# Optimization experiments

Measured on AMD Instinct MI355X. Metric: run time of the kernel, lower is better.

The kernel has to match this reference:

```python
import jax, jax.numpy as jnp
from jax import lax
import numpy as np

# ---- static config (matches init_kwargs) ----
B, H, W = 8, 32, 32
L = H * W                      # 1024 tokens
D_MODEL = 384
MAMBA_DIM = 192                # d_model * d_mamba_ratio
LOCAL_DIM = 192
D_INNER = 384                  # expand_m * MAMBA_DIM
D_STATE = 16
D_CONV = 4
DT_RANK = 12                   # ceil(MAMBA_DIM / 16)
NDIR = 4                       # h, h_flip, v, v_flip
RED = 48                       # int(D_INNER * 0.125), BiAttn reduce dim
INNER_C = 192                  # LOCAL_DIM * expand_c
K_C = 8                        # local block depthwise kernel size


def setup_inputs() -> dict:
    key = jax.random.key(0)
    ks = jax.random.split(key, 16)
    s = 0.02
    return {
        "x": jax.random.normal(ks[0], (B, L, D_MODEL), jnp.float32),
        "in_proj_w": jax.random.normal(ks[1], (2 * D_INNER, MAMBA_DIM)) * s,
        "A_log": jnp.broadcast_to(jnp.log(jnp.arange(1, D_STATE + 1, dtype=jnp.float32)), (NDIR, D_INNER, D_STATE)) + 0.0,
        "conv_w": jax.random.normal(ks[2], (NDIR, D_INNER, D_CONV)) * 0.2,
        "conv_b": jax.random.normal(ks[3], (NDIR, D_INNER)) * 0.02,
        "xproj_w": jax.random.normal(ks[4], (NDIR, DT_RANK + 2 * D_STATE, D_INNER)) * s,
        "dtproj_w": jax.random.normal(ks[5], (NDIR, D_INNER, DT_RANK)) * (DT_RANK ** -0.5),
        "dtproj_b": jax.random.normal(ks[6], (NDIR, D_INNER)) * 0.5 - 4.0,
        "Dp": jnp.ones((NDIR, D_INNER)),
        "out_proj_w": jax.random.normal(ks[7], (MAMBA_DIM, D_INNER)) * s,
        "attn_ln_g": jnp.ones((D_INNER,)),
        "attn_ln_b": jnp.zeros((D_INNER,)),
        "attn_gr_w": jax.random.normal(ks[8], (RED, D_INNER)) * s,
        "attn_gr_b": jnp.zeros((RED,)),
        "attn_cs_w": jax.random.normal(ks[9], (D_INNER, RED)) * s,
        "attn_cs_b": jnp.zeros((D_INNER,)),
        "pw1_w": jax.random.normal(ks[10], (2 * INNER_C, LOCAL_DIM)) * s,
        "pw1_b": jnp.zeros((2 * INNER_C,)),
        "dw_w": jax.random.normal(ks[11], (INNER_C, K_C)) * 0.2,
        "dw_b": jnp.zeros((INNER_C,)),
        "bn_g": jnp.ones((INNER_C,)),
        "bn_b": jnp.zeros((INNER_C,)),
        "pw2_w": jax.random.normal(ks[12], (LOCAL_DIM, INNER_C)) * s,
        "pw2_b": jnp.zeros((LOCAL_DIM,)),
    }


def _forward(x, in_proj_w, A_log, conv_w, conv_b, xproj_w, dtproj_w, dtproj_b, Dp,
             out_proj_w, attn_ln_g, attn_ln_b, attn_gr_w, attn_gr_b, attn_cs_w, attn_cs_b,
             pw1_w, pw1_b, dw_w, dw_b, bn_g, bn_b, pw2_w, pw2_b):
    mamba_in = x[:, :, :MAMBA_DIM]
    local_in = x[:, :, MAMBA_DIM:]

    # ---------- MultiMamba branch ----------
    xz = jnp.swapaxes(mamba_in @ in_proj_w.T, 1, 2)   # (B, 2*D_INNER, L)

    def to_dir(t, i):
        # reorder channel-last-token axis per scan direction
        if i == 0:
            return t
        if i == 1:
            return jnp.flip(t, -1)
        tv = t.reshape(B, -1, H, W).swapaxes(-1, -2).reshape(B, -1, L)  # column-major scan
        return tv if i == 2 else jnp.flip(tv, -1)

    def from_dir(t, i):
        if i == 0:
            return t
        if i == 1:
            return jnp.flip(t, -1)
        if i == 3:
            t = jnp.flip(t, -1)
        return t.reshape(B, -1, W, H).swapaxes(-1, -2).reshape(B, -1, L)

    def ssm_dir(xzd, i):
        # mamba_inner_fn_no_out_proj: causal dwconv -> silu -> x_proj -> selective scan -> gate
        xp, z = jnp.split(xzd, 2, axis=1)            # (B, D_INNER, L) each
        xpad = jnp.pad(xp, ((0, 0), (0, 0), (D_CONV - 1, 0)))
        u = lax.conv_general_dilated(xpad, conv_w[i][:, None, :], (1,), 'VALID',
                                     dimension_numbers=('NCH', 'OIH', 'NCH'),
                                     feature_group_count=D_INNER)
        u = jax.nn.silu(u + conv_b[i][None, :, None])
        dbl = jnp.einsum('bdl,rd->brl', u, xproj_w[i])
        dt = dbl[:, :DT_RANK]
        Bm = dbl[:, DT_RANK:DT_RANK + D_STATE]
        Cm = dbl[:, DT_RANK + D_STATE:]
        delta = jax.nn.softplus(jnp.einsum('brl,dr->bdl', dt, dtproj_w[i]) + dtproj_b[i][None, :, None])
        A = -jnp.exp(A_log[i])                        # (D_INNER, D_STATE)

        def step(h, inps):
            d_t, B_t, C_t, u_t = inps                 # (B,d),(B,n),(B,n),(B,d)
            h = jnp.exp(d_t[:, :, None] * A) * h + (d_t * u_t)[:, :, None] * B_t[:, None, :]
            return h, jnp.einsum('bdn,bn->bd', h, C_t)

        h0 = jnp.zeros((B, D_INNER, D_STATE), x.dtype)
        _, ys = lax.scan(step, h0, (delta.transpose(2, 0, 1), Bm.transpose(2, 0, 1),
                                    Cm.transpose(2, 0, 1), u.transpose(2, 0, 1)))
        y = ys.transpose(1, 2, 0) + u * Dp[i][:, None]  # (B, D_INNER, L)
        return y * jax.nn.silu(z)

    def biattn(t):                                     # (B, L, D_INNER)
        mu = t.mean(-1, keepdims=True)
        var = ((t - mu) ** 2).mean(-1, keepdims=True)
        tn = (t - mu) / jnp.sqrt(var + 1e-5) * attn_ln_g + attn_ln_b
        g = tn.mean(1, keepdims=True)                  # global pool (B,1,D_INNER)
        g = jax.nn.gelu(g @ attn_gr_w.T + attn_gr_b, approximate=False)
        c = jax.nn.sigmoid(g @ attn_cs_w.T + attn_cs_b)
        return t * c

    acc = jnp.zeros((B, L, D_INNER), x.dtype)
    for i in range(NDIR):                              # fixed small set of directions
        out_i = from_dir(ssm_dir(to_dir(xz, i), i), i)
        acc = acc + biattn(jnp.swapaxes(out_i, 1, 2))
    mamba_out = acc @ out_proj_w.T                     # (B, L, MAMBA_DIM)

    # ---------- Local conv branch ----------
    hch = jnp.einsum('blc,oc->bol', local_in, pw1_w) + pw1_b[None, :, None]
    a, gte = jnp.split(hch, 2, axis=1)
    hch = a * jax.nn.sigmoid(gte)                      # GLU, (B, INNER_C, L)
    pad_l = K_C // 2
    pad_r = K_C // 2 - (K_C + 1) % 2                   # calc_same_padding(8) -> (4, 3)
    hpad = jnp.pad(hch, ((0, 0), (0, 0), (pad_l, pad_r)))
    hch = lax.conv_general_dilated(hpad, dw_w[:, None, :], (1,), 'VALID',
                                   dimension_numbers=('NCH', 'OIH', 'NCH'),
                                   feature_group_count=INNER_C) + dw_b[None, :, None]
    mu = hch.mean((0, 2))                              # BatchNorm1d (training-mode batch stats)
    var = hch.var((0, 2))
    hch = (hch - mu[None, :, None]) / jnp.sqrt(var + 1e-5)[None, :, None] * bn_g[None, :, None] + bn_b[None, :, None]
    hch = hch * jax.nn.sigmoid(hch)                    # Swish
    local_out = jnp.einsum('bcl,oc->blo', hch, pw2_w) + pw2_b

    return jnp.concatenate([mamba_out, local_out], axis=-1)


def reference(x, in_proj_w, A_log, conv_w, conv_b, xproj_w, dtproj_w, dtproj_b, Dp,
              out_proj_w, attn_ln_g, attn_ln_b, attn_gr_w, attn_gr_b, attn_cs_w, attn_cs_b,
              pw1_w, pw1_b, dw_w, dw_b, bn_g, bn_b, pw2_w, pw2_b):
    return _forward(x, in_proj_w, A_log, conv_w, conv_b, xproj_w, dtproj_w, dtproj_b, Dp,
                    out_proj_w, attn_ln_g, attn_ln_b, attn_gr_w, attn_gr_b, attn_cs_w, attn_cs_b,
                    pw1_w, pw1_b, dw_w, dw_b, bn_g, bn_b, pw2_w, pw2_b)
```

## Files before the change

kernel.cpp:

```cpp
#include <hip/hip_runtime.h>
#include <stdint.h>


#define DEV __device__ __forceinline__

typedef __attribute__((ext_vector_type(8))) short short8;
typedef __attribute__((ext_vector_type(4))) short short4v;
typedef __attribute__((ext_vector_type(4))) float f32x4;

DEV float bf(ushort v) { union { uint32_t u; float f; } c; c.u = ((uint32_t)v) << 16; return c.f; }
DEV ushort fbf(float f) {
  union { float f; uint32_t u; } c; c.f = f;
  uint32_t u = c.u;
  return (ushort)((u + 0x7FFFu + ((u >> 16) & 1u)) >> 16);
}

#if __has_builtin(__builtin_amdgcn_exp2f)
DEV float fexp2(float x) { return __builtin_amdgcn_exp2f(x); }
#else
DEV float fexp2(float x) { return __expf(x * 0.6931471805599453f); }
#endif

template<int CTRL>
DEV float rradd(float x) {
  return x + __int_as_float(__builtin_amdgcn_update_dpp(
      0, __float_as_int(x), CTRL, 0xF, 0xF, true));
}

DEV int pmap(int i, int j) {
  if (i == 0) return j;
  if (i == 1) return 1023 - j;
  if (i == 2) return ((j & 31) << 5) | (j >> 5);
  int k = 1023 - j; return ((k & 31) << 5) | (k >> 5);
}

DEV void cvt4(const float* __restrict__ s, ushort* __restrict__ d, int blk, int tid) {
  const int idx = (blk * 256 + tid) * 4;
  float4 v = *(const float4*)(s + idx);
  d[idx] = fbf(v.x); d[idx + 1] = fbf(v.y); d[idx + 2] = fbf(v.z); d[idx + 3] = fbf(v.w);
}

__global__ __launch_bounds__(256) void prep_all(
    const float* __restrict__ x, ushort* __restrict__ xb,
    const float* __restrict__ ipw, ushort* __restrict__ ipwb,
    const float* __restrict__ opw, ushort* __restrict__ opwb,
    const float* __restrict__ pw1w, ushort* __restrict__ pw1wb,
    const float* __restrict__ pw2w, ushort* __restrict__ pw2wb,
    const float* __restrict__ xw, ushort* __restrict__ xwp)
{
  const int bx = blockIdx.x, tid = threadIdx.x;
  if (bx < 3072)      cvt4(x, xb, bx, tid);
  else if (bx < 3216) cvt4(ipw, ipwb, bx - 3072, tid);
  else if (bx < 3288) cvt4(opw, opwb, bx - 3216, tid);
  else if (bx < 3360) cvt4(pw1w, pw1wb, bx - 3288, tid);
  else if (bx < 3396) cvt4(pw2w, pw2wb, bx - 3360, tid);
  else {
    const int row = bx - 3396;
    const int i = row >> 6, nn = row & 63;
    for (int c = tid; c < 384; c += 256)
      xwp[(size_t)row * 384 + c] = (nn < 44) ? fbf(xw[((size_t)i * 44 + nn) * 384 + c]) : (ushort)0;
  }
}

template<bool BF16OUT, bool BIAS>
__global__ __launch_bounds__(256) void gemm_bt(
    const ushort* __restrict__ A, long long sAz, int lda,
    const ushort* __restrict__ Bw, long long sBz,
    const float* __restrict__ bias,
    void* __restrict__ C, long long sCz, int ldc, int coff, int K)
{
  __shared__ ushort As[64][40];
  __shared__ ushort Bs[64][40];
  A += (size_t)blockIdx.z * sAz;
  Bw += (size_t)blockIdx.z * sBz;
  const int tid = threadIdx.x;
  const int m0 = blockIdx.x * 64, n0 = blockIdx.y * 64;
  const int w = tid >> 6, lane = tid & 63, l15 = lane & 15, quad = lane >> 4;
  const int sr = tid >> 2, sc = (tid & 3) * 8;
  f32x4 acc[4] = {};
  for (int k0 = 0; k0 < K; k0 += 32) {
    __syncthreads();
    *(short8*)&As[sr][sc] = *(const short8*)(A + (size_t)(m0 + sr) * lda + k0 + sc);
    *(short8*)&Bs[sr][sc] = *(const short8*)(Bw + (size_t)(n0 + sr) * K + k0 + sc);
    __syncthreads();
    short8 av = *(short8*)&As[w * 16 + l15][quad * 8];
#pragma unroll
    for (int nt = 0; nt < 4; nt++) {
      short8 bv = *(short8*)&Bs[nt * 16 + l15][quad * 8];
      acc[nt] = __builtin_amdgcn_mfma_f32_16x16x32_bf16(av, bv, acc[nt], 0, 0, 0);
    }
  }
  float* cf = (float*)C + (size_t)blockIdx.z * sCz;
  ushort* cb = (ushort*)C + (size_t)blockIdx.z * sCz;
#pragma unroll
  for (int nt = 0; nt < 4; nt++) {
    const int col = n0 + nt * 16 + l15;
    const float bv = BIAS ? bias[col] : 0.f;
#pragma unroll
    for (int r = 0; r < 4; r++) {
      const int row = m0 + w * 16 + quad * 4 + r;
      float v = acc[nt][r] + bv;
      if (BF16OUT) cb[(size_t)row * ldc + coff + col] = fbf(v);
      else         cf[(size_t)row * ldc + coff + col] = v;
    }
  }
}

__global__ __launch_bounds__(256) void gemm_dual(
    const ushort* __restrict__ A0, int lda0, const ushort* __restrict__ B0,
    const float* __restrict__ bias0, void* __restrict__ C0, int ldc0, int coff0, int K0,
    int nt0, int bf0,
    const ushort* __restrict__ A1, int lda1, const ushort* __restrict__ B1,
    const float* __restrict__ bias1, void* __restrict__ C1, int ldc1, int coff1, int K1,
    int bf1, float* __restrict__ bnsum)
{
  __shared__ ushort As[64][40];
  __shared__ ushort Bs[64][40];
  if (blockIdx.x == 0 && blockIdx.y == 0) {
    for (int k = threadIdx.x; k < 384; k += 256) bnsum[k] = 0.f;
  }
  const ushort* A; const ushort* Bw; const float* bias; void* C;
  int lda, ldc, coff, K, bf16o, n0;
  if ((int)blockIdx.y < nt0) {
    A = A0; lda = lda0; Bw = B0; bias = bias0; C = C0; ldc = ldc0; coff = coff0; K = K0;
    bf16o = bf0; n0 = blockIdx.y * 64;
  } else {
    A = A1; lda = lda1; Bw = B1; bias = bias1; C = C1; ldc = ldc1; coff = coff1; K = K1;
    bf16o = bf1; n0 = (blockIdx.y - nt0) * 64;
  }
  const int tid = threadIdx.x;
  const int m0 = blockIdx.x * 64;
  const int w = tid >> 6, lane = tid & 63, l15 = lane & 15, quad = lane >> 4;
  const int sr = tid >> 2, sc = (tid & 3) * 8;
  f32x4 acc[4] = {};
  for (int k0 = 0; k0 < K; k0 += 32) {
    __syncthreads();
    *(short8*)&As[sr][sc] = *(const short8*)(A + (size_t)(m0 + sr) * lda + k0 + sc);
    *(short8*)&Bs[sr][sc] = *(const short8*)(Bw + (size_t)(n0 + sr) * K + k0 + sc);
    __syncthreads();
    short8 av = *(short8*)&As[w * 16 + l15][quad * 8];
#pragma unroll
    for (int nt = 0; nt < 4; nt++) {
      short8 bv = *(short8*)&Bs[nt * 16 + l15][quad * 8];
      acc[nt] = __builtin_amdgcn_mfma_f32_16x16x32_bf16(av, bv, acc[nt], 0, 0, 0);
    }
  }
#pragma unroll
  for (int nt = 0; nt < 4; nt++) {
    const int col = n0 + nt * 16 + l15;
    const float bv = bias ? bias[col] : 0.f;
#pragma unroll
    for (int r = 0; r < 4; r++) {
      const int row = m0 + w * 16 + quad * 4 + r;
      float v = acc[nt][r] + bv;
      if (bf16o) ((ushort*)C)[(size_t)row * ldc + coff + col] = fbf(v);
      else       ((float*)C)[(size_t)row * ldc + coff + col] = v;
    }
  }
}

__global__ __launch_bounds__(256) void gemm_pw2(
    const float* __restrict__ h2, const float* __restrict__ bnsum,
    const float* __restrict__ bng, const float* __restrict__ bnb,
    const ushort* __restrict__ Bw, const float* __restrict__ bias,
    float* __restrict__ C)
{
  __shared__ ushort As[64][40];
  __shared__ ushort Bs[64][40];
  __shared__ float bsc[192], bsh[192];
  const int tid = threadIdx.x;
  const int m0 = blockIdx.x * 64, n0 = blockIdx.y * 64;
  const int w = tid >> 6, lane = tid & 63, l15 = lane & 15, quad = lane >> 4;
  const int sr = tid >> 2, sc = (tid & 3) * 8;
  for (int cth = tid; cth < 192; cth += 256) {
    float m = bnsum[cth] * (1.f / 8192.f);
    float va = bnsum[192 + cth] * (1.f / 8192.f) - m * m;
    float s = bng[cth] * rsqrtf(va + 1e-5f);
    bsc[cth] = s; bsh[cth] = bnb[cth] - m * s;
  }
  f32x4 acc[4] = {};
  for (int k0 = 0; k0 < 192; k0 += 32) {
    __syncthreads();
    {
      const float* hr = h2 + (size_t)(m0 + sr) * 192 + k0 + sc;
      f32x4 a0 = *(const f32x4*)(hr);
      f32x4 a1 = *(const f32x4*)(hr + 4);
      short8 v;
#pragma unroll
      for (int k = 0; k < 8; k++) {
        const float xx = (k < 4) ? a0[k] : a1[k - 4];
        const float xn = xx * bsc[k0 + sc + k] + bsh[k0 + sc + k];
        v[k] = (short)fbf(xn / (1.f + __expf(-xn)));
      }
      *(short8*)&As[sr][sc] = v;
    }
    *(short8*)&Bs[sr][sc] = *(const short8*)(Bw + (size_t)(n0 + sr) * 192 + k0 + sc);
    __syncthreads();
    short8 av = *(short8*)&As[w * 16 + l15][quad * 8];
#pragma unroll
    for (int nt = 0; nt < 4; nt++) {
      short8 bv = *(short8*)&Bs[nt * 16 + l15][quad * 8];
      acc[nt] = __builtin_amdgcn_mfma_f32_16x16x32_bf16(av, bv, acc[nt], 0, 0, 0);
    }
  }
#pragma unroll
  for (int nt = 0; nt < 4; nt++) {
    const int col = n0 + nt * 16 + l15;
    const float bv = bias[col];
#pragma unroll
    for (int r = 0; r < 4; r++) {
      const int row = m0 + w * 16 + quad * 4 + r;
      C[(size_t)row * 384 + 192 + col] = acc[nt][r] + bv;
    }
  }
}

__global__ __launch_bounds__(256) void convdbl_kernel(
    const ushort* __restrict__ xzb, const float* __restrict__ cw,
    const float* __restrict__ cb, const ushort* __restrict__ xwp,
    ushort* __restrict__ u, float* __restrict__ dbl)
{
  __shared__ __align__(16) ushort sxz[67][392];
  __shared__ float swt[384][4];
  __shared__ float scb[384];
  const int tid = threadIdx.x;
  const int i = blockIdx.y;
  const int m0 = blockIdx.x * 64;
  const int b = m0 >> 10, j0 = m0 & 1023;

  for (int k = tid; k < 1536; k += 256) ((float*)swt)[k] = cw[(size_t)i * 1536 + k];
  for (int k = tid; k < 384; k += 256) scb[k] = cb[i * 384 + k];
  for (int g = tid; g < 67 * 96; g += 256) {
    const int rr = g / 96, c4 = (g % 96) * 4;
    const int jj = j0 - 3 + rr;
    short4v v = {};
    if (jj >= 0)
      v = *(const short4v*)(xzb + (size_t)((b << 10) + pmap(i, jj)) * 768 + c4);
    *(short4v*)&sxz[rr][c4] = v;
  }
  __syncthreads();
  {
    const int r = tid >> 2, cp = tid & 3;
    ushort* ur = u + ((size_t)((i * 8 + b) << 10) + j0 + r) * 384 + cp * 96;
#pragma unroll 4
    for (int q = 0; q < 24; q++) {
      const int c = cp * 96 + q * 4;
      const short4v x0 = *(const short4v*)&sxz[r + 0][c];
      const short4v x1 = *(const short4v*)&sxz[r + 1][c];
      const short4v x2 = *(const short4v*)&sxz[r + 2][c];
      const short4v x3 = *(const short4v*)&sxz[r + 3][c];
      short4v o;
#pragma unroll
      for (int j = 0; j < 4; j++) {
        const f32x4 wv = *(const f32x4*)&swt[c + j][0];
        float s = bf((ushort)x0[j]) * wv[0] + bf((ushort)x1[j]) * wv[1]
                + bf((ushort)x2[j]) * wv[2] + bf((ushort)x3[j]) * wv[3] + scb[c + j];
        o[j] = (short)fbf(s / (1.f + __expf(-s)));
      }
      *(short4v*)(ur + q * 4) = o;
    }
  }
  ushort (*As)[40] = (ushort(*)[40])&sxz[0][0];
  ushort (*Bs)[40] = (ushort(*)[40])(&sxz[0][0] + 2560);
  const ushort* Au = u + (size_t)i * 8192 * 384;
  const ushort* Bw = xwp + (size_t)i * 64 * 384;
  const int w = tid >> 6, lane = tid & 63, l15 = lane & 15, quad = lane >> 4;
  const int sr = tid >> 2, sc = (tid & 3) * 8;
  f32x4 acc[4] = {};
  for (int k0 = 0; k0 < 384; k0 += 32) {
    __syncthreads();
    *(short8*)&As[sr][sc] = *(const short8*)(Au + (size_t)(m0 + sr) * 384 + k0 + sc);
    *(short8*)&Bs[sr][sc] = *(const short8*)(Bw + (size_t)sr * 384 + k0 + sc);
    __syncthreads();
    short8 av = *(short8*)&As[w * 16 + l15][quad * 8];
#pragma unroll
    for (int nt = 0; nt < 4; nt++) {
      short8 bv = *(short8*)&Bs[nt * 16 + l15][quad * 8];
      acc[nt] = __builtin_amdgcn_mfma_f32_16x16x32_bf16(av, bv, acc[nt], 0, 0, 0);
    }
  }
  float* cf = dbl + (size_t)i * 8192 * 64;
#pragma unroll
  for (int nt = 0; nt < 4; nt++) {
    const int col = nt * 16 + l15;
#pragma unroll
    for (int r = 0; r < 4; r++) {
      const int row = m0 + w * 16 + quad * 4 + r;
      cf[(size_t)row * 64 + col] = acc[nt][r];
    }
  }
}

#define NCH 16
#define CJ 64
__global__ __launch_bounds__(256, 3) void scan9_kernel(
    const ushort* __restrict__ u,
    const float*  __restrict__ dbl,
    const ushort* __restrict__ xzb,
    const float* __restrict__ alog, const float* __restrict__ dtw,
    const float* __restrict__ dtb, const float* __restrict__ Dpw,
    ushort* __restrict__ y)
{
  const int dt0 = blockIdx.x * NCH;
  const int b = blockIdx.y, i = blockIdx.z;
  const int tid = threadIdx.x;
  const int ch = tid >> 4, n = tid & 15;
  const int srow = tid >> 2, role = tid & 3;

  __shared__ float sbc[CJ / 2][68];
  __shared__ float sdu[CJ / 2][68];
  __shared__ float sy[CJ][20];
  __shared__ float sDp[NCH];

  float w48[4][12], dtbv4[4];
#pragma unroll
  for (int cc = 0; cc < 4; cc++) {
    const int chp = 4 * role + cc;
#pragma unroll
    for (int r = 0; r < 12; r++) w48[cc][r] = dtw[((size_t)i * 384 + dt0 + chp) * 12 + r];
    dtbv4[cc] = dtb[i * 384 + dt0 + chp];
  }
  const float L2E = 1.4426950408889634f;
  const float Al = -__expf(alog[((size_t)i * 384 + dt0 + ch) * 16 + n]) * L2E;
  if (tid < NCH) sDp[tid] = Dpw[i * 384 + dt0 + tid];

  const float selm[4] = { (n >> 2) == 0 ? 1.f : 0.f, (n >> 2) == 1 ? 1.f : 0.f,
                          (n >> 2) == 2 ? 1.f : 0.f, (n >> 2) == 3 ? 1.f : 0.f };

  const size_t rb = (size_t)(i * 8 + b) << 10;
  const ushort* ub = u + rb * 384 + dt0;
  const float* dblb = dbl + rb * 64;
  const ushort* zb = xzb + ((size_t)b << 10) * 768 + 384 + dt0;
  ushort* yb = y + rb * 384 + dt0;
  const float* sdup = &sdu[0][4 * ch];
  const float* sbcp = &sbc[0][4 * n];

  f32x4 nd0, nd1, nd2, ns0, ns1, ns2; short4v nu, nz;
  {
    const float* src = dblb + (size_t)srow * 64;
    nd0 = *(const f32x4*)(src); nd1 = *(const f32x4*)(src + 4); nd2 = *(const f32x4*)(src + 8);
    const float* seg = src + role * 12;
    ns0 = *(const f32x4*)(seg); ns1 = *(const f32x4*)(seg + 4); ns2 = *(const f32x4*)(seg + 8);
    nu = *(const short4v*)(ub + (size_t)srow * 384 + 4 * role);
    nz = *(const short4v*)(zb + (size_t)pmap(i, srow) * 768 + 4 * role);
  }

  float h = 0.f;

  for (int c = 0; c < 16; c++) {
    const int j0 = c * CJ;
    f32x4 uf, zf;
#pragma unroll
    for (int k = 0; k < 4; k++) { uf[k] = bf((ushort)nu[k]); zf[k] = bf((ushort)nz[k]); }
    if (role != 0) {
      float vals[12];
#pragma unroll
      for (int k = 0; k < 4; k++) { vals[k] = ns0[k]; vals[4 + k] = ns1[k]; vals[8 + k] = ns2[k]; }
#pragma unroll
      for (int k = 0; k < 12; k++) {
        const int f = role * 12 + k;
        if (f < 44) {
          const int isC = (f >= 28) ? 1 : 0;
          const int nn = isC ? (f - 28) : (f - 12);
          sbc[srow >> 1][4 * nn + 2 * (srow & 1) + isC] = vals[k];
        }
      }
    }
    {
      float dtr[12];
#pragma unroll
      for (int k = 0; k < 4; k++) { dtr[k] = nd0[k]; dtr[4 + k] = nd1[k]; dtr[8 + k] = nd2[k]; }
#pragma unroll
      for (int cc = 0; cc < 4; cc++) {
        float s = dtbv4[cc];
#pragma unroll
        for (int r = 0; r < 12; r++) s += dtr[r] * w48[cc][r];
        const float dl = fmaxf(s, 0.f) + __logf(1.f + __expf(-fabsf(s)));
        float2 pr; pr.x = dl; pr.y = dl * uf[cc];
        *(float2*)&sdu[srow >> 1][4 * (4 * role + cc) + 2 * (srow & 1)] = pr;
      }
    }
    __syncthreads();
    {
      const int cn = (c < 15) ? (c + 1) : 0;
      const int rown = cn * CJ + srow;
      const float* src = dblb + (size_t)rown * 64;
      nd0 = *(const f32x4*)(src); nd1 = *(const f32x4*)(src + 4); nd2 = *(const f32x4*)(src + 8);
      const float* seg = src + role * 12;
      ns0 = *(const f32x4*)(seg); ns1 = *(const f32x4*)(seg + 4); ns2 = *(const f32x4*)(seg + 8);
      nu = *(const short4v*)(ub + (size_t)rown * 384 + 4 * role);
      nz = *(const short4v*)(zb + (size_t)pmap(i, rown) * 768 + 4 * role);
    }
#pragma unroll
    for (int q = 0; q < 4; q++) {
      f32x4 pq = {0.f, 0.f, 0.f, 0.f};
#pragma unroll
      for (int s2 = 0; s2 < 8; s2++) {
        const f32x4 duP = *(const f32x4*)(sdup + (q * 8 + s2) * 68);
        const f32x4 bcP = *(const f32x4*)(sbcp + (q * 8 + s2) * 68);
        {
          const float e = fexp2(duP[0] * Al);
          h = e * h + duP[1] * bcP[0];
          float p = h * bcP[1];
          p = rradd<0x124>(p); p = rradd<0x128>(p);
          pq[s2 >> 1] = fmaf(selm[(2 * s2) & 3], p, pq[s2 >> 1]);
        }
        {
          const float e = fexp2(duP[2] * Al);
          h = e * h + duP[3] * bcP[2];
          float p = h * bcP[3];
          p = rradd<0x124>(p); p = rradd<0x128>(p);
          pq[s2 >> 1] = fmaf(selm[(2 * s2 + 1) & 3], p, pq[s2 >> 1]);
        }
      }
#pragma unroll
      for (int j = 0; j < 4; j++) {
        float t2 = rradd<0xB1>(pq[j]);
        t2 = rradd<0x4E>(t2);
        if ((n & 3) == 0) sy[(q << 4) | (j << 2) | (n >> 2)][ch] = t2;
      }
    }
    __syncthreads();
    {
      const int lo = pmap(i, j0 + srow);
      const f32x4 y4 = *(const f32x4*)&sy[srow][role * 4];
      short4v o;
#pragma unroll
      for (int t = 0; t < 4; t++) {
        const float z = zf[t];
        const float val = (y4[t] + uf[t] * sDp[role * 4 + t]) * (z / (1.f + __expf(-z)));
        o[t] = (short)fbf(val);
      }
      *(short4v*)(yb + (size_t)lo * 384 + role * 4) = o;
    }
  }
}

__global__ __launch_bounds__(256) void lngm_kernel(const ushort* __restrict__ y,
                                                   float* __restrict__ G16)
{
  const int slab = blockIdx.x, b = blockIdx.y, i = blockIdx.z;
  const int tid = threadIdx.x;
  const int w = tid >> 6, lane = tid & 63;
  __shared__ float smu[64], srs[64];
  __shared__ ushort sy16[64][384];
  const size_t base = (size_t)i * 8192 + b * 1024 + slab * 64;
  for (int rr = 0; rr < 16; rr++) {
    const int r = w * 16 + rr;
    const ushort* yr = y + (base + r) * 384;
    const short4v v4 = *(const short4v*)(yr + 4 * lane);
    const uint32_t v2 = *(const uint32_t*)(yr + 256 + 2 * lane);
    *(short4v*)&sy16[r][4 * lane] = v4;
    *(uint32_t*)&sy16[r][256 + 2 * lane] = v2;
    float s = 0.f, ss = 0.f;
#pragma unroll
    for (int t = 0; t < 4; t++) { float v = bf((ushort)v4[t]); s += v; ss += v * v; }
    { float v = bf((ushort)(v2 & 0xffffu)); s += v; ss += v * v; }
    { float v = bf((ushort)(v2 >> 16));     s += v; ss += v * v; }
#pragma unroll
    for (int off = 1; off < 64; off <<= 1) { s += __shfl_xor(s, off, 64); ss += __shfl_xor(ss, off, 64); }
    if (lane == 0) {
      float m = s * (1.f / 384.f);
      float va = ss * (1.f / 384.f) - m * m;
      smu[r] = m;
      srs[r] = rsqrtf(va + 1e-5f);
    }
  }
  __syncthreads();
  if (tid < 192) {
    const int c0 = tid * 2;
    float s0 = 0.f, s1 = 0.f;
#pragma unroll 8
    for (int r = 0; r < 64; r++) {
      const uint32_t pv = *(const uint32_t*)&sy16[r][c0];
      const float rs = srs[r], mu = smu[r];
      s0 += (bf((ushort)(pv & 0xffffu)) - mu) * rs;
      s1 += (bf((ushort)(pv >> 16)) - mu) * rs;
    }
    float* g = G16 + ((size_t)(i * 8 + b) * 16 + slab) * 384 + c0;
    g[0] = s0; g[1] = s1;
  }
}

__global__ __launch_bounds__(384) void gate_kernel(const float* __restrict__ G16,
    const float* __restrict__ lng, const float* __restrict__ lnb,
    const float* __restrict__ grw, const float* __restrict__ grb,
    const float* __restrict__ csw, const float* __restrict__ csb, float* __restrict__ cbuf)
{
  const int b = blockIdx.x, i = blockIdx.y;
  const int ib = i * 8 + b;
  const int t = threadIdx.x;
  __shared__ float sG[384];
  __shared__ float g48[48];
  {
    const float* g = G16 + (size_t)ib * 16 * 384 + t;
    float s = 0.f;
#pragma unroll
    for (int k = 0; k < 16; k++) s += g[k * 384];
    sG[t] = s * (1.f / 1024.f) * lng[t] + lnb[t];
  }
  __syncthreads();
  {
    const int row = t >> 3, seg = t & 7;
    const float* wr = grw + (size_t)row * 384 + seg * 48;
    const float* gr = sG + seg * 48;
    float s = 0.f;
#pragma unroll
    for (int k = 0; k < 48; k++) s += gr[k] * wr[k];
    s += __shfl_xor(s, 1, 64); s += __shfl_xor(s, 2, 64); s += __shfl_xor(s, 4, 64);
    if (seg == 0) {
      s += grb[row];
      g48[row] = 0.5f * s * (1.f + erff(s * 0.70710678118f));
    }
  }
  __syncthreads();
  {
    float s = csb[t];
#pragma unroll
    for (int r = 0; r < 48; r++) s += g48[r] * csw[(size_t)t * 48 + r];
    cbuf[(size_t)ib * 384 + t] = 1.f / (1.f + __expf(-s));
  }
}

__global__ __launch_bounds__(384) void accgate_kernel(const ushort* __restrict__ y,
    const float* __restrict__ cbuf, ushort* __restrict__ accb)
{
  const int t = threadIdx.x;
  const int row = blockIdx.x * 4 + (t / 96);
  const int cg = (t % 96) * 4;
  const int b = row >> 10;
  f32x4 s = {};
#pragma unroll
  for (int i = 0; i < 4; i++) {
    const short4v v = *(const short4v*)(y + ((size_t)i * 8192 + row) * 384 + cg);
    const f32x4 cv = *(const f32x4*)(cbuf + (size_t)(i * 8 + b) * 384 + cg);
#pragma unroll
    for (int k = 0; k < 4; k++) s[k] += bf((ushort)v[k]) * cv[k];
  }
  short4v o;
#pragma unroll
  for (int k = 0; k < 4; k++) o[k] = (short)fbf(s[k]);
  *(short4v*)(accb + (size_t)row * 384 + cg) = o;
}

__global__ __launch_bounds__(192) void gludwbn_kernel(const ushort* __restrict__ hchb,
    const float* __restrict__ dww, const float* __restrict__ dwb,
    float* __restrict__ h2, float* __restrict__ bnsum)
{
  const int c = threadIdx.x;
  const int lt = blockIdx.x, b = blockIdx.y;
  __shared__ float sv[23][192];
  const int l0 = lt * 16;
#pragma unroll 4
  for (int r = 0; r < 23; r++) {
    const int ls = l0 + r - 4;
    float v = 0.f;
    if (ls >= 0 && ls < 1024) {
      const size_t rr = (size_t)((b << 10) + ls) * 384;
      const float a = bf(hchb[rr + c]);
      const float g = bf(hchb[rr + 192 + c]);
      v = a / (1.f + __expf(-g));
    }
    sv[r][c] = v;
  }
  __syncthreads();
  float wk[8];
#pragma unroll
  for (int k = 0; k < 8; k++) wk[k] = dww[(c << 3) + k];
  const float bias = dwb[c];
  float sacc = 0.f, ssacc = 0.f;
  for (int q = 0; q < 16; q++) {
    float s = bias;
#pragma unroll
    for (int k = 0; k < 8; k++) s += sv[q + k][c] * wk[k];
    h2[(size_t)((b << 10) + l0 + q) * 192 + c] = s;
    sacc += s; ssacc += s * s;
  }
  atomicAdd(&bnsum[c], sacc);
  atomicAdd(&bnsum[192 + c], ssacc);
}

extern "C" void kernel_launch(void* const* d_in, const int* in_sizes, int n_in,
                              void* d_out, int out_size, void* d_ws, size_t ws_size,
                              hipStream_t stream) {
  const float* x    = (const float*)d_in[0];
  const float* ipw  = (const float*)d_in[1];
  const float* alog = (const float*)d_in[2];
  const float* cw   = (const float*)d_in[3];
  const float* cbv  = (const float*)d_in[4];
  const float* xw   = (const float*)d_in[5];
  const float* dtw  = (const float*)d_in[6];
  const float* dtb  = (const float*)d_in[7];
  const float* Dpw  = (const float*)d_in[8];
  const float* opw  = (const float*)d_in[9];
  const float* lng  = (const float*)d_in[10];
  const float* lnb  = (const float*)d_in[11];
  const float* grw  = (const float*)d_in[12];
  const float* grb  = (const float*)d_in[13];
  const float* csw  = (const float*)d_in[14];
  const float* csb  = (const float*)d_in[15];
  const float* pw1w = (const float*)d_in[16];
  const float* pw1b = (const float*)d_in[17];
  const float* dww  = (const float*)d_in[18];
  const float* dwb  = (const float*)d_in[19];
  const float* bng  = (const float*)d_in[20];
  const float* bnb  = (const float*)d_in[21];
  const float* pw2w = (const float*)d_in[22];
  const float* pw2b = (const float*)d_in[23];
  float* out = (float*)d_out;

  char* ws = (char*)d_ws;
  ushort* xb    = (ushort*)(ws + 0);
  ushort* xzb   = (ushort*)(ws + 6291456);
  ushort* u     = (ushort*)(ws + 18874368);
  float*  dbl   = (float*)(ws + 44040192);
  ushort* y     = (ushort*)(ws + 52428800);
  ushort* accb  = (ushort*)(ws + 77594624);
  float*  G16   = (float*)(ws + 83886080);
  float*  cbuf  = (float*)(ws + 84672512);
  ushort* xwp   = (ushort*)(ws + 84721664);
  ushort* ipwb  = (ushort*)(ws + 84918272);
  ushort* opwb  = (ushort*)(ws + 85213184);
  ushort* pw1wb = (ushort*)(ws + 85360640);
  ushort* pw2wb = (ushort*)(ws + 85508096);
  float*  bnsum = (float*)(ws + 85581824);
  ushort* hchb = (ushort*)(ws + 18874368);
  float*  h2   = (float*)(ws + 34603008);

  prep_all<<<dim3(3652), 256, 0, stream>>>(x, xb, ipw, ipwb, opw, opwb,
                                           pw1w, pw1wb, pw2w, pw2wb, xw, xwp);
  gemm_bt<true, false><<<dim3(128, 12, 1), 256, 0, stream>>>(
      xb, 0, 384, ipwb, 0, nullptr, xzb, 0, 768, 0, 192);
  convdbl_kernel<<<dim3(128, 4), 256, 0, stream>>>(xzb, cw, cbv, xwp, u, dbl);
  scan9_kernel<<<dim3(24, 8, 4), 256, 0, stream>>>(u, dbl, xzb, alog, dtw, dtb, Dpw, y);
  lngm_kernel<<<dim3(16, 8, 4), 256, 0, stream>>>(y, G16);
  gate_kernel<<<dim3(8, 4), 384, 0, stream>>>(G16, lng, lnb, grw, grb, csw, csb, cbuf);
  accgate_kernel<<<dim3(2048), 384, 0, stream>>>(y, cbuf, accb);
  gemm_dual<<<dim3(128, 9), 256, 0, stream>>>(
      accb, 384, opwb, nullptr, out, 384, 0, 384, 3, 0,
      xb + 192, 384, pw1wb, pw1b, hchb, 384, 0, 192, 1, bnsum);
  gludwbn_kernel<<<dim3(64, 8), 192, 0, stream>>>(hchb, dww, dwb, h2, bnsum);
  gemm_pw2<<<dim3(128, 3), 256, 0, stream>>>(h2, bnsum, bng, bnb, pw2wb, pw2b, out);
}
```

Before: 312.0 us.

## Retile projection GEMMs to 32x192 blocks so each A tile is loaded once

The three projection GEMMs move from 64x64 output tiles to 32-row by 192-column tiles, with each wave computing six 16x16 MFMA tiles. A rows are now read from global memory once per 192-wide column span instead of once per 64-wide span, which matters most for gemm_pw2, where the BN+Swish transform of h2 is no longer recomputed three times. The cost is that B-weight traffic per block triples, while block count goes to 1024 for the in-projection, 768 for the dual GEMM and 256 for pw2. Each wave also holds six accumulators and reads six B fragments per A fragment.

```diff
diff --git a/kernel.cpp b/kernel.cpp
--- a/kernel.cpp
+++ b/kernel.cpp
@@ -63,98 +63,105 @@
 }
 
 template<bool BF16OUT, bool BIAS>
-__global__ __launch_bounds__(256) void gemm_bt(
-    const ushort* __restrict__ A, long long sAz, int lda,
-    const ushort* __restrict__ Bw, long long sBz,
+__global__ __launch_bounds__(256) void gemm_w192(
+    const ushort* __restrict__ A, int lda,
+    const ushort* __restrict__ Bw,
     const float* __restrict__ bias,
-    void* __restrict__ C, long long sCz, int ldc, int coff, int K)
-{
-  __shared__ ushort As[64][40];
-  __shared__ ushort Bs[64][40];
-  A += (size_t)blockIdx.z * sAz;
-  Bw += (size_t)blockIdx.z * sBz;
+    void* __restrict__ C, int ldc, int K)
+{
+  __shared__ ushort As[32][40];
+  __shared__ ushort Bs[192][40];
   const int tid = threadIdx.x;
-  const int m0 = blockIdx.x * 64, n0 = blockIdx.y * 64;
+  const int m0 = blockIdx.x * 32, n0 = blockIdx.y * 192;
   const int w = tid >> 6, lane = tid & 63, l15 = lane & 15, quad = lane >> 4;
-  const int sr = tid >> 2, sc = (tid & 3) * 8;
-  f32x4 acc[4] = {};
+  const int mrow = (w & 1) * 16, ntb = (w >> 1) * 6;
+  const int brow = tid >> 2, bcol = (tid & 3) * 8;
+  f32x4 acc[6] = {};
   for (int k0 = 0; k0 < K; k0 += 32) {
     __syncthreads();
-    *(short8*)&As[sr][sc] = *(const short8*)(A + (size_t)(m0 + sr) * lda + k0 + sc);
-    *(short8*)&Bs[sr][sc] = *(const short8*)(Bw + (size_t)(n0 + sr) * K + k0 + sc);
-    __syncthreads();
-    short8 av = *(short8*)&As[w * 16 + l15][quad * 8];
-#pragma unroll
-    for (int nt = 0; nt < 4; nt++) {
-      short8 bv = *(short8*)&Bs[nt * 16 + l15][quad * 8];
-      acc[nt] = __builtin_amdgcn_mfma_f32_16x16x32_bf16(av, bv, acc[nt], 0, 0, 0);
-    }
-  }
-  float* cf = (float*)C + (size_t)blockIdx.z * sCz;
-  ushort* cb = (ushort*)C + (size_t)blockIdx.z * sCz;
-#pragma unroll
-  for (int nt = 0; nt < 4; nt++) {
-    const int col = n0 + nt * 16 + l15;
+    if (tid < 128)
+      *(short8*)&As[brow][bcol] = *(const short8*)(A + (size_t)(m0 + brow) * lda + k0 + bcol);
+#pragma unroll
+    for (int rr = 0; rr < 3; rr++)
+      *(short8*)&Bs[brow + rr * 64][bcol] =
+          *(const short8*)(Bw + (size_t)(n0 + brow + rr * 64) * K + k0 + bcol);
+    __syncthreads();
+    short8 av = *(short8*)&As[mrow + l15][quad * 8];
+#pragma unroll
+    for (int j = 0; j < 6; j++) {
+      short8 bv = *(short8*)&Bs[(ntb + j) * 16 + l15][quad * 8];
+      acc[j] = __builtin_amdgcn_mfma_f32_16x16x32_bf16(av, bv, acc[j], 0, 0, 0);
+    }
+  }
+  float* cf = (float*)C;
+  ushort* cb = (ushort*)C;
+#pragma unroll
+  for (int j = 0; j < 6; j++) {
+    const int col = n0 + (ntb + j) * 16 + l15;
     const float bv = BIAS ? bias[col] : 0.f;
 #pragma unroll
     for (int r = 0; r < 4; r++) {
-      const int row = m0 + w * 16 + quad * 4 + r;
-      float v = acc[nt][r] + bv;
-      if (BF16OUT) cb[(size_t)row * ldc + coff + col] = fbf(v);
-      else         cf[(size_t)row * ldc + coff + col] = v;
-    }
-  }
-}
-
-__global__ __launch_bounds__(256) void gemm_dual(
+      const int row = m0 + mrow + quad * 4 + r;
+      float v = acc[j][r] + bv;
+      if (BF16OUT) cb[(size_t)row * ldc + col] = fbf(v);
+      else         cf[(size_t)row * ldc + col] = v;
+    }
+  }
+}
+
+__global__ __launch_bounds__(256) void gemm_dual192(
     const ushort* __restrict__ A0, int lda0, const ushort* __restrict__ B0,
-    const float* __restrict__ bias0, void* __restrict__ C0, int ldc0, int coff0, int K0,
-    int nt0, int bf0,
+    void* __restrict__ C0, int ldc0, int K0, int bf0,
     const ushort* __restrict__ A1, int lda1, const ushort* __restrict__ B1,
-    const float* __restrict__ bias1, void* __restrict__ C1, int ldc1, int coff1, int K1,
-    int bf1, float* __restrict__ bnsum)
-{
-  __shared__ ushort As[64][40];
-  __shared__ ushort Bs[64][40];
+    const float* __restrict__ bias1,
+    void* __restrict__ C1, int ldc1, int K1, int bf1, float* __restrict__ bnsum)
+{
+  __shared__ ushort As[32][40];
+  __shared__ ushort Bs[192][40];
   if (blockIdx.x == 0 && blockIdx.y == 0) {
     for (int k = threadIdx.x; k < 384; k += 256) bnsum[k] = 0.f;
   }
   const ushort* A; const ushort* Bw; const float* bias; void* C;
-  int lda, ldc, coff, K, bf16o, n0;
-  if ((int)blockIdx.y < nt0) {
-    A = A0; lda = lda0; Bw = B0; bias = bias0; C = C0; ldc = ldc0; coff = coff0; K = K0;
-    bf16o = bf0; n0 = blockIdx.y * 64;
+  int lda, ldc, K, bf16o, n0;
+  if (blockIdx.y == 0) {
+    A = A0; lda = lda0; Bw = B0; bias = nullptr; C = C0; ldc = ldc0; K = K0;
+    bf16o = bf0; n0 = 0;
   } else {
-    A = A1; lda = lda1; Bw = B1; bias = bias1; C = C1; ldc = ldc1; coff = coff1; K = K1;
-    bf16o = bf1; n0 = (blockIdx.y - nt0) * 64;
+    A = A1; lda = lda1; Bw = B1; bias = bias1; C = C1; ldc = ldc1; K = K1;
+    bf16o = bf1; n0 = (blockIdx.y - 1) * 192;
   }
   const int tid = threadIdx.x;
-  const int m0 = blockIdx.x * 64;
+  const int m0 = blockIdx.x * 32;
   const int w = tid >> 6, lane = tid & 63, l15 = lane & 15, quad = lane >> 4;
-  const int sr = tid >> 2, sc = (tid & 3) * 8;
-  f32x4 acc[4] = {};
+  const int mrow = (w & 1) * 16, ntb = (w >> 1) * 6;
+  const int brow = tid >> 2, bcol = (tid & 3) * 8;
+  f32x4 acc[6] = {};
   for (int k0 = 0; k0 < K; k0 += 32) {
     __syncthreads();
-    *(short8*)&As[sr][sc] = *(const short8*)(A + (size_t)(m0 + sr) * lda + k0 + sc);
-    *(short8*)&Bs[sr][sc] = *(const short8*)(Bw + (size_t)(n0 + sr) * K + k0 + sc);
-    __syncthreads();
-    short8 av = *(short8*)&As[w * 16 + l15][quad * 8];
-#pragma unroll
-    for (int nt = 0; nt < 4; nt++) {
-      short8 bv = *(short8*)&Bs[nt * 16 + l15][quad * 8];
-      acc[nt] = __builtin_amdgcn_mfma_f32_16x16x32_bf16(av, bv, acc[nt], 0, 0, 0);
-    }
-  }
-#pragma unroll
-  for (int nt = 0; nt < 4; nt++) {
-    const int col = n0 + nt * 16 + l15;
+    if (tid < 128)
+      *(short8*)&As[brow][bcol] = *(const short8*)(A + (size_t)(m0 + brow) * lda + k0 + bcol);
+#pragma unroll
+    for (int rr = 0; rr < 3; rr++)
+      *(short8*)&Bs[brow + rr * 64][bcol] =
+          *(const short8*)(Bw + (size_t)(n0 + brow + rr * 64) * K + k0 + bcol);
+    __syncthreads();
+    short8 av = *(short8*)&As[mrow + l15][quad * 8];
+#pragma unroll
+    for (int j = 0; j < 6; j++) {
+      short8 bv = *(short8*)&Bs[(ntb + j) * 16 + l15][quad * 8];
+      acc[j] = __builtin_amdgcn_mfma_f32_16x16x32_bf16(av, bv, acc[j], 0, 0, 0);
+    }
+  }
+#pragma unroll
+  for (int j = 0; j < 6; j++) {
+    const int col = n0 + (ntb + j) * 16 + l15;
     const float bv = bias ? bias[col] : 0.f;
 #pragma unroll
     for (int r = 0; r < 4; r++) {
-      const int row = m0 + w * 16 + quad * 4 + r;
-      float v = acc[nt][r] + bv;
-      if (bf16o) ((ushort*)C)[(size_t)row * ldc + coff + col] = fbf(v);
-      else       ((float*)C)[(size_t)row * ldc + coff + col] = v;
+      const int row = m0 + mrow + quad * 4 + r;
+      float v = acc[j][r] + bv;
+      if (bf16o) ((ushort*)C)[(size_t)row * ldc + col] = fbf(v);
+      else       ((float*)C)[(size_t)row * ldc + col] = v;
     }
   }
 }
@@ -165,52 +172,56 @@
     const ushort* __restrict__ Bw, const float* __restrict__ bias,
     float* __restrict__ C)
 {
-  __shared__ ushort As[64][40];
-  __shared__ ushort Bs[64][40];
+  __shared__ ushort As[32][40];
+  __shared__ ushort Bs[192][40];
   __shared__ float bsc[192], bsh[192];
   const int tid = threadIdx.x;
-  const int m0 = blockIdx.x * 64, n0 = blockIdx.y * 64;
+  const int m0 = blockIdx.x * 32;
   const int w = tid >> 6, lane = tid & 63, l15 = lane & 15, quad = lane >> 4;
-  const int sr = tid >> 2, sc = (tid & 3) * 8;
-  for (int cth = tid; cth < 192; cth += 256) {
-    float m = bnsum[cth] * (1.f / 8192.f);
-    float va = bnsum[192 + cth] * (1.f / 8192.f) - m * m;
-    float s = bng[cth] * rsqrtf(va + 1e-5f);
-    bsc[cth] = s; bsh[cth] = bnb[cth] - m * s;
-  }
-  f32x4 acc[4] = {};
+  const int mrow = (w & 1) * 16, ntb = (w >> 1) * 6;
+  const int brow = tid >> 2, bcol = (tid & 3) * 8;
+  if (tid < 192) {
+    float m = bnsum[tid] * (1.f / 8192.f);
+    float va = bnsum[192 + tid] * (1.f / 8192.f) - m * m;
+    float s = bng[tid] * rsqrtf(va + 1e-5f);
+    bsc[tid] = s; bsh[tid] = bnb[tid] - m * s;
+  }
+  f32x4 acc[6] = {};
   for (int k0 = 0; k0 < 192; k0 += 32) {
     __syncthreads();
-    {
-      const float* hr = h2 + (size_t)(m0 + sr) * 192 + k0 + sc;
+    if (tid < 128) {
+      const float* hr = h2 + (size_t)(m0 + brow) * 192 + k0 + bcol;
       f32x4 a0 = *(const f32x4*)(hr);
       f32x4 a1 = *(const f32x4*)(hr + 4);
       short8 v;
 #pragma unroll
       for (int k = 0; k < 8; k++) {
         const float xx = (k < 4) ? a0[k] : a1[k - 4];
-        const float xn = xx * bsc[k0 + sc + k] + bsh[k0 + sc + k];
+        const float xn = xx * bsc[k0 + bcol + k] + bsh[k0 + bcol + k];
         v[k] = (short)fbf(xn / (1.f + __expf(-xn)));
       }
-      *(short8*)&As[sr][sc] = v;
-    }
-    *(short8*)&Bs[sr][sc] = *(const short8*)(Bw + (size_t)(n0 + sr) * 192 + k0 + sc);
-    __syncthreads();
-    short8 av = *(short8*)&As[w * 16 + l15][quad * 8];
-#pragma unroll
-    for (int nt = 0; nt < 4; nt++) {
-      short8 bv = *(short8*)&Bs[nt * 16 + l15][quad * 8];
-      acc[nt] = __builtin_amdgcn_mfma_f32_16x16x32_bf16(av, bv, acc[nt], 0, 0, 0);
-    }
-  }
-#pragma unroll
-  for (int nt = 0; nt < 4; nt++) {
-    const int col = n0 + nt * 16 + l15;
+      *(short8*)&As[brow][bcol] = v;
+    }
+#pragma unroll
+    for (int rr = 0; rr < 3; rr++)
+      *(short8*)&Bs[brow + rr * 64][bcol] =
+          *(const short8*)(Bw + (size_t)(brow + rr * 64) * 192 + k0 + bcol);
+    __syncthreads();
+    short8 av = *(short8*)&As[mrow + l15][quad * 8];
+#pragma unroll
+    for (int j = 0; j < 6; j++) {
+      short8 bv = *(short8*)&Bs[(ntb + j) * 16 + l15][quad * 8];
+      acc[j] = __builtin_amdgcn_mfma_f32_16x16x32_bf16(av, bv, acc[j], 0, 0, 0);
+    }
+  }
+#pragma unroll
+  for (int j = 0; j < 6; j++) {
+    const int col = (ntb + j) * 16 + l15;
     const float bv = bias[col];
 #pragma unroll
     for (int r = 0; r < 4; r++) {
-      const int row = m0 + w * 16 + quad * 4 + r;
-      C[(size_t)row * 384 + 192 + col] = acc[nt][r] + bv;
+      const int row = m0 + mrow + quad * 4 + r;
+      C[(size_t)row * 384 + 192 + col] = acc[j][r] + bv;
     }
   }
 }
@@ -629,16 +640,16 @@
 
   prep_all<<<dim3(3652), 256, 0, stream>>>(x, xb, ipw, ipwb, opw, opwb,
                                            pw1w, pw1wb, pw2w, pw2wb, xw, xwp);
-  gemm_bt<true, false><<<dim3(128, 12, 1), 256, 0, stream>>>(
-      xb, 0, 384, ipwb, 0, nullptr, xzb, 0, 768, 0, 192);
+  gemm_w192<true, false><<<dim3(256, 4), 256, 0, stream>>>(
+      xb, 384, ipwb, nullptr, xzb, 768, 192);
   convdbl_kernel<<<dim3(128, 4), 256, 0, stream>>>(xzb, cw, cbv, xwp, u, dbl);
   scan9_kernel<<<dim3(24, 8, 4), 256, 0, stream>>>(u, dbl, xzb, alog, dtw, dtb, Dpw, y);
   lngm_kernel<<<dim3(16, 8, 4), 256, 0, stream>>>(y, G16);
   gate_kernel<<<dim3(8, 4), 384, 0, stream>>>(G16, lng, lnb, grw, grb, csw, csb, cbuf);
   accgate_kernel<<<dim3(2048), 384, 0, stream>>>(y, cbuf, accb);
-  gemm_dual<<<dim3(128, 9), 256, 0, stream>>>(
-      accb, 384, opwb, nullptr, out, 384, 0, 384, 3, 0,
-      xb + 192, 384, pw1wb, pw1b, hchb, 384, 0, 192, 1, bnsum);
+  gemm_dual192<<<dim3(256, 3), 256, 0, stream>>>(
+      accb, 384, opwb, out, 384, 384, 0,
+      xb + 192, 384, pw1wb, pw1b, hchb, 384, 192, 1, bnsum);
   gludwbn_kernel<<<dim3(64, 8), 192, 0, stream>>>(hchb, dww, dwb, h2, bnsum);
-  gemm_pw2<<<dim3(128, 3), 256, 0, stream>>>(h2, bnsum, bng, bnb, pw2wb, pw2b, out);
-}
+  gemm_pw2<<<dim3(256), 256, 0, stream>>>(h2, bnsum, bng, bnb, pw2wb, pw2b, out);
+}
```

New measurement: 315.5 us. About the same (+1.1%).

## Fuse direction-gate accumulation into out_proj GEMM A-tile loading

Applied to the files above, without the earlier changes.

Removes the separate accgate kernel by computing the gated sum over the four direction outputs directly while staging the A tile of the out_proj GEMM. The accb intermediate is no longer written to and reread from global memory. The dual GEMM is also retiled to 32-row by 192-column blocks with six MFMA accumulators per wave. The trade-off is that only half the threads load A, with a four-way reduction on the load path, and B tiles are larger.

```diff
diff --git a/kernel.cpp b/kernel.cpp
--- a/kernel.cpp
+++ b/kernel.cpp
@@ -106,55 +106,76 @@
   }
 }
 
-__global__ __launch_bounds__(256) void gemm_dual(
-    const ushort* __restrict__ A0, int lda0, const ushort* __restrict__ B0,
-    const float* __restrict__ bias0, void* __restrict__ C0, int ldc0, int coff0, int K0,
-    int nt0, int bf0,
-    const ushort* __restrict__ A1, int lda1, const ushort* __restrict__ B1,
-    const float* __restrict__ bias1, void* __restrict__ C1, int ldc1, int coff1, int K1,
-    int bf1, float* __restrict__ bnsum)
-{
-  __shared__ ushort As[64][40];
-  __shared__ ushort Bs[64][40];
+__global__ __launch_bounds__(256) void gemm_dualfuse(
+    const ushort* __restrict__ yv, const float* __restrict__ cbuf,
+    const ushort* __restrict__ B0, float* __restrict__ C0,
+    const ushort* __restrict__ A1, const ushort* __restrict__ B1,
+    const float* __restrict__ bias1, ushort* __restrict__ C1,
+    float* __restrict__ bnsum)
+{
+  __shared__ ushort As[32][40];
+  __shared__ ushort Bs[192][40];
+  __shared__ float scb[4 * 384];
   if (blockIdx.x == 0 && blockIdx.y == 0) {
     for (int k = threadIdx.x; k < 384; k += 256) bnsum[k] = 0.f;
   }
-  const ushort* A; const ushort* Bw; const float* bias; void* C;
-  int lda, ldc, coff, K, bf16o, n0;
-  if ((int)blockIdx.y < nt0) {
-    A = A0; lda = lda0; Bw = B0; bias = bias0; C = C0; ldc = ldc0; coff = coff0; K = K0;
-    bf16o = bf0; n0 = blockIdx.y * 64;
+  const int tid = threadIdx.x;
+  const int m0 = blockIdx.x * 32;
+  const int w = tid >> 6, lane = tid & 63, l15 = lane & 15, quad = lane >> 4;
+  const int mrow = (w & 1) * 16, ntb = (w >> 1) * 6;
+  const int brow = tid >> 2, bcol = (tid & 3) * 8;
+  const int cfg0 = (blockIdx.y == 0);
+  const int b = m0 >> 10;
+  const ushort* Bw; int K, n0;
+  if (cfg0) {
+    Bw = B0; K = 384; n0 = 0;
+    for (int k = tid; k < 1536; k += 256)
+      scb[k] = cbuf[(size_t)((k / 384) * 8 + b) * 384 + (k % 384)];
   } else {
-    A = A1; lda = lda1; Bw = B1; bias = bias1; C = C1; ldc = ldc1; coff = coff1; K = K1;
-    bf16o = bf1; n0 = (blockIdx.y - nt0) * 64;
-  }
-  const int tid = threadIdx.x;
-  const int m0 = blockIdx.x * 64;
-  const int w = tid >> 6, lane = tid & 63, l15 = lane & 15, quad = lane >> 4;
-  const int sr = tid >> 2, sc = (tid & 3) * 8;
-  f32x4 acc[4] = {};
+    Bw = B1; K = 192; n0 = (blockIdx.y - 1) * 192;
+  }
+  f32x4 acc[6] = {};
   for (int k0 = 0; k0 < K; k0 += 32) {
     __syncthreads();
-    *(short8*)&As[sr][sc] = *(const short8*)(A + (size_t)(m0 + sr) * lda + k0 + sc);
-    *(short8*)&Bs[sr][sc] = *(const short8*)(Bw + (size_t)(n0 + sr) * K + k0 + sc);
-    __syncthreads();
-    short8 av = *(short8*)&As[w * 16 + l15][quad * 8];
-#pragma unroll
-    for (int nt = 0; nt < 4; nt++) {
-      short8 bv = *(short8*)&Bs[nt * 16 + l15][quad * 8];
-      acc[nt] = __builtin_amdgcn_mfma_f32_16x16x32_bf16(av, bv, acc[nt], 0, 0, 0);
-    }
-  }
-#pragma unroll
-  for (int nt = 0; nt < 4; nt++) {
-    const int col = n0 + nt * 16 + l15;
-    const float bv = bias ? bias[col] : 0.f;
+    if (tid < 128) {
+      const int row = m0 + brow, kc = k0 + bcol;
+      if (cfg0) {
+        float a8[8] = {};
+#pragma unroll
+        for (int i = 0; i < 4; i++) {
+          const short8 v = *(const short8*)(yv + ((size_t)i * 8192 + row) * 384 + kc);
+          const float* cv = &scb[i * 384 + kc];
+#pragma unroll
+          for (int k = 0; k < 8; k++) a8[k] += bf((ushort)v[k]) * cv[k];
+        }
+        short8 o;
+#pragma unroll
+        for (int k = 0; k < 8; k++) o[k] = (short)fbf(a8[k]);
+        *(short8*)&As[brow][bcol] = o;
+      } else {
+        *(short8*)&As[brow][bcol] = *(const short8*)(A1 + (size_t)row * 384 + kc);
+      }
+    }
+#pragma unroll
+    for (int rr = 0; rr < 3; rr++)
+      *(short8*)&Bs[brow + rr * 64][bcol] =
+          *(const short8*)(Bw + (size_t)(n0 + brow + rr * 64) * K + k0 + bcol);
+    __syncthreads();
+    short8 av = *(short8*)&As[mrow + l15][quad * 8];
+#pragma unroll
+    for (int j = 0; j < 6; j++) {
+      short8 bv = *(short8*)&Bs[(ntb + j) * 16 + l15][quad * 8];
+      acc[j] = __builtin_amdgcn_mfma_f32_16x16x32_bf16(av, bv, acc[j], 0, 0, 0);
+    }
+  }
+#pragma unroll
+  for (int j = 0; j < 6; j++) {
+    const int col = n0 + (ntb + j) * 16 + l15;
 #pragma unroll
     for (int r = 0; r < 4; r++) {
-      const int row = m0 + w * 16 + quad * 4 + r;
-      float v = acc[nt][r] + bv;
-      if (bf16o) ((ushort*)C)[(size_t)row * ldc + coff + col] = fbf(v);
-      else       ((float*)C)[(size_t)row * ldc + coff + col] = v;
+      const int row = m0 + mrow + quad * 4 + r;
+      if (cfg0) C0[(size_t)row * 384 + col] = acc[j][r];
+      else      C1[(size_t)row * 384 + col] = fbf(acc[j][r] + bias1[col]);
     }
   }
 }
@@ -520,27 +541,6 @@
     for (int r = 0; r < 48; r++) s += g48[r] * csw[(size_t)t * 48 + r];
     cbuf[(size_t)ib * 384 + t] = 1.f / (1.f + __expf(-s));
   }
-}
-
-__global__ __launch_bounds__(384) void accgate_kernel(const ushort* __restrict__ y,
-    const float* __restrict__ cbuf, ushort* __restrict__ accb)
-{
-  const int t = threadIdx.x;
-  const int row = blockIdx.x * 4 + (t / 96);
-  const int cg = (t % 96) * 4;
-  const int b = row >> 10;
-  f32x4 s = {};
-#pragma unroll
-  for (int i = 0; i < 4; i++) {
-    const short4v v = *(const short4v*)(y + ((size_t)i * 8192 + row) * 384 + cg);
-    const f32x4 cv = *(const f32x4*)(cbuf + (size_t)(i * 8 + b) * 384 + cg);
-#pragma unroll
-    for (int k = 0; k < 4; k++) s[k] += bf((ushort)v[k]) * cv[k];
-  }
-  short4v o;
-#pragma unroll
-  for (int k = 0; k < 4; k++) o[k] = (short)fbf(s[k]);
-  *(short4v*)(accb + (size_t)row * 384 + cg) = o;
 }
 
 __global__ __launch_bounds__(192) void gludwbn_kernel(const ushort* __restrict__ hchb,
@@ -615,7 +615,6 @@
   ushort* u     = (ushort*)(ws + 18874368);
   float*  dbl   = (float*)(ws + 44040192);
   ushort* y     = (ushort*)(ws + 52428800);
-  ushort* accb  = (ushort*)(ws + 77594624);
   float*  G16   = (float*)(ws + 83886080);
   float*  cbuf  = (float*)(ws + 84672512);
   ushort* xwp   = (ushort*)(ws + 84721664);
@@ -635,10 +634,8 @@
   scan9_kernel<<<dim3(24, 8, 4), 256, 0, stream>>>(u, dbl, xzb, alog, dtw, dtb, Dpw, y);
   lngm_kernel<<<dim3(16, 8, 4), 256, 0, stream>>>(y, G16);
   gate_kernel<<<dim3(8, 4), 384, 0, stream>>>(G16, lng, lnb, grw, grb, csw, csb, cbuf);
-  accgate_kernel<<<dim3(2048), 384, 0, stream>>>(y, cbuf, accb);
-  gemm_dual<<<dim3(128, 9), 256, 0, stream>>>(
-      accb, 384, opwb, nullptr, out, 384, 0, 384, 3, 0,
-      xb + 192, 384, pw1wb, pw1b, hchb, 384, 0, 192, 1, bnsum);
+  gemm_dualfuse<<<dim3(256, 3), 256, 0, stream>>>(
+      y, cbuf, opwb, out, xb + 192, pw1wb, pw1b, hchb, bnsum);
   gludwbn_kernel<<<dim3(64, 8), 192, 0, stream>>>(hchb, dww, dwb, h2, bnsum);
   gemm_pw2<<<dim3(128, 3), 256, 0, stream>>>(h2, bnsum, bng, bnb, pw2wb, pw2b, out);
 }
```

Measured after the change: 312.4 us. About the same (+0.1%).
